# Optimization experiments

Hardware: AMD Instinct MI355X
Metric: run time of the kernel (lower is better)

The kernel has to match this reference:

```python
import jax, jax.numpy as jnp
import numpy as np

B, N, C, P, H = 4096, 14, 512, 1024, 8  # batch, seq(=seg_sz), in_ch, proj_ch, heads
D = P // H                               # dim_head = 128
SCALE = D ** -0.5
EPS = 1e-5


def setup_inputs() -> dict:
    key = jax.random.key(0)
    ks = jax.random.split(key, 12)
    inp = {
        "x1": jax.random.normal(ks[0], (B, N, C), jnp.float32),
        "x2": jax.random.normal(ks[1], (B, N, C), jnp.float32),
        # hr: external per-batch gate over attention scores, broadcast over heads
        "hr": jax.random.uniform(ks[2], (B, N, N), jnp.float32),
        # Embedding(in_ch*2 -> proj_ch-256), modeled as Linear
        "W_emb": jax.random.normal(ks[3], (2 * C, P - 256), jnp.float32) * (2 * C) ** -0.5,
        "b_emb": jnp.zeros((P - 256,), jnp.float32),
        # learned absolute positional embedding [N, 256]
        "pos": jax.random.normal(ks[4], (N, 256), jnp.float32) * 0.02,
        # qkv projection, no bias (bias=False in source)
        "W_qkv": jax.random.normal(ks[5], (P, 3 * P), jnp.float32) * P ** -0.5,
        # post-attention LayerNorm
        "ln_g": jnp.ones((P,), jnp.float32),
        "ln_b": jnp.zeros((P,), jnp.float32),
        # FeedForward(P -> 1.5P -> P)
        "W1": jax.random.normal(ks[6], (P, int(P * 1.5)), jnp.float32) * P ** -0.5,
        "b1": jnp.zeros((int(P * 1.5),), jnp.float32),
        "W2": jax.random.normal(ks[7], (int(P * 1.5), P), jnp.float32) * (int(P * 1.5)) ** -0.5,
        "b2": jnp.zeros((P,), jnp.float32),
    }
    return inp


def _layernorm(x, g, b):
    mu = jnp.mean(x, axis=-1, keepdims=True)
    var = jnp.mean(jnp.square(x - mu), axis=-1, keepdims=True)
    return (x - mu) * jax.lax.rsqrt(var + EPS) * g + b


def reference(x1, x2, hr, W_emb, b_emb, pos, W_qkv, ln_g, ln_b, W1, b1, W2, b2):
    x = jnp.concatenate([x1, x2], axis=-1)                    # [B,N,2C]
    e = x @ W_emb + b_emb                                     # [B,N,P-256]
    pe = jnp.broadcast_to(pos, (x.shape[0],) + pos.shape)     # [B,N,256]
    x = jnp.concatenate([e, pe], axis=-1)                     # [B,N,P]
    res = x
    qkv = x @ W_qkv                                           # [B,N,3P]
    q, k, v = jnp.split(qkv, 3, axis=-1)
    def split_heads(t):
        return t.reshape(t.shape[0], t.shape[1], H, D).transpose(0, 2, 1, 3)  # [B,H,N,D]
    q, k, v = split_heads(q), split_heads(k), split_heads(v)
    dots = jnp.einsum('bhid,bhjd->bhij', q, k) * SCALE        # [B,H,N,N]
    attn = jax.nn.softmax(dots, axis=-1) * hr[:, None]        # post-softmax multiplicative gate
    # dropout = identity (eval mode)
    o = jnp.einsum('bhij,bhjd->bhid', attn, v)                # [B,H,N,D]
    o = o.transpose(0, 2, 1, 3).reshape(o.shape[0], N, P)     # [B,N,P]
    x = _layernorm(o + res, ln_g, ln_b)
    x = jax.nn.gelu(x @ W1 + b1) @ W2 + b2                    # FeedForward (dropout=identity)
    return x
```

## Files before the change

### kernel.cpp

```cpp
#include <hip/hip_runtime.h>
#include <hip/hip_bf16.h>
#include <cstdint>
#include <cstddef>

using bf16 = __hip_bfloat16;

typedef __attribute__((ext_vector_type(8))) short short8;
typedef __attribute__((ext_vector_type(4))) float fx4;

#define MROWS 57344

__device__ __forceinline__ float b2f(bf16 v) { return __bfloat162float(v); }
__device__ __forceinline__ bf16  f2b(float v) { return __float2bfloat16(v); }

union U2B { uint2 u; bf16 h[4]; };
union U4B { uint4 u; bf16 h[8]; };

#define GL2LDS(g, l)                                                  \
  __builtin_amdgcn_global_load_lds(                                   \
      (__attribute__((address_space(1))) void*)(g),                   \
      (__attribute__((address_space(3))) void*)(l), 16, 0, 0)

__global__ void detect_k(const uint32_t* __restrict__ g, int* __restrict__ flag) {
  if (threadIdx.x == 0) *flag = ((g[0] & 0xFFFFu) == 0x3F80u) ? 1 : 0;
}

__device__ __forceinline__ float loadAs(const void* p, size_t i, bool isbf) {
  return isbf ? b2f(((const bf16*)p)[i]) : ((const float*)p)[i];
}

__global__ void cvt8_k(const void* __restrict__ src, bf16* __restrict__ dst,
                       int n8, const int* __restrict__ flag) {
  const int i = blockIdx.x * 256 + threadIdx.x;
  if (i >= n8) return;
  U4B o;
  if (*flag) {
    o.u = ((const uint4*)src)[i];
  } else {
    const float* f = (const float*)src + (size_t)i * 8;
#pragma unroll
    for (int j = 0; j < 8; ++j) o.h[j] = f2b(f[j]);
  }
  ((uint4*)dst)[i] = o.u;
}

__global__ void transpose_k(const void* __restrict__ W, bf16* __restrict__ Wt,
                            int K, int N, const int* __restrict__ flag) {
  __shared__ float s[32][33];
  const bool isbf = (*flag != 0);
  const int n0 = blockIdx.x * 32, k0 = blockIdx.y * 32;
  const int tx = threadIdx.x, ty = threadIdx.y;
  for (int i = ty; i < 32; i += 8)
    s[i][tx] = loadAs(W, (size_t)(k0 + i) * N + n0 + tx, isbf);
  __syncthreads();
  for (int i = ty; i < 32; i += 8)
    Wt[(size_t)(n0 + i) * K + k0 + tx] = f2b(s[tx][i]);
}

__global__ void concat_k(const void* __restrict__ x1, const void* __restrict__ x2,
                         bf16* __restrict__ xcat, const int* __restrict__ flag) {
  const int m = blockIdx.x, j = threadIdx.x;
  const bool isbf = (*flag != 0);
  const void* src = (j < 64) ? x1 : x2;
  const int jj = (j < 64) ? j : j - 64;
  U4B o;
  if (isbf) {
    o.u = *(const uint4*)((const bf16*)src + (size_t)m * 512 + jj * 8);
  } else {
    const float* f = (const float*)src + (size_t)m * 512 + jj * 8;
#pragma unroll
    for (int q = 0; q < 8; ++q) o.h[q] = f2b(f[q]);
  }
  *(uint4*)(xcat + (size_t)m * 1024 + j * 8) = o.u;
}

__global__ void posfill_k(const void* __restrict__ pos, bf16* __restrict__ xp,
                          const int* __restrict__ flag) {
  const int m = blockIdx.x, j = threadIdx.x;
  xp[(size_t)m * 1024 + 768 + j] = f2b(loadAs(pos, (m % 14) * 256 + j, *flag != 0));
}

template <int EPI, int OUTDT>
__global__ __launch_bounds__(256, 2)
void gemm_bt(const bf16* __restrict__ A, const bf16* __restrict__ Bt,
             void* __restrict__ C, const bf16* __restrict__ bias,
             const int* __restrict__ dtflag, int M, int N, int K, int ldc) {
  __shared__ bf16 smem[16384];
  bf16* a_s = smem;
  bf16* b_s = smem + 8192;

  const int t = threadIdx.x;
  const int w = t >> 6, L = t & 63, quad = L >> 4, l15 = L & 15;
  const int wr = w >> 1, wc = w & 1;
  const int m0 = blockIdx.y * 128, n0 = blockIdx.x * 128;
  const bool bfout = OUTDT ? (*dtflag != 0) : true;

  const int srow = L >> 2;
  const int scol = (L & 3) * 8;
  const bf16* gA = A + (size_t)(m0 + w * 32 + srow) * K + scol;
  const bf16* gB = Bt + (size_t)(n0 + w * 32 + srow) * K + scol;
  const size_t gstep = (size_t)16 * K;

  fx4 acc[4][4];
#pragma unroll
  for (int r = 0; r < 4; ++r)
#pragma unroll
    for (int c = 0; c < 4; ++c) acc[r][c] = fx4{0.f, 0.f, 0.f, 0.f};

  {
    bf16* lA = a_s + w * 1024;
    bf16* lB = b_s + w * 1024;
    GL2LDS(gA, lA);
    GL2LDS(gA + gstep, lA + 512);
    GL2LDS(gB, lB);
    GL2LDS(gB + gstep, lB + 512);
  }

  int cur = 0;
  for (int k0 = 0; k0 < K; k0 += 32) {
    const int nk = k0 + 32;
    if (nk < K) {
      bf16* lA = a_s + (cur ^ 1) * 4096 + w * 1024;
      bf16* lB = b_s + (cur ^ 1) * 4096 + w * 1024;
      GL2LDS(gA + nk, lA);
      GL2LDS(gA + gstep + nk, lA + 512);
      GL2LDS(gB + nk, lB);
      GL2LDS(gB + gstep + nk, lB + 512);
      asm volatile("s_waitcnt vmcnt(4)" ::: "memory");
    } else {
      asm volatile("s_waitcnt vmcnt(0)" ::: "memory");
    }
    __builtin_amdgcn_s_barrier();

    const bf16* as = a_s + cur * 4096;
    const bf16* bs = b_s + cur * 4096;
    short8 af[4], bfr[4];
#pragma unroll
    for (int r = 0; r < 4; ++r)
      af[r] = *(const short8*)(as + (wr * 64 + r * 16 + l15) * 32 + quad * 8);
#pragma unroll
    for (int c = 0; c < 4; ++c)
      bfr[c] = *(const short8*)(bs + (wc * 64 + c * 16 + l15) * 32 + quad * 8);
    asm volatile("s_waitcnt lgkmcnt(0)" ::: "memory");
    __builtin_amdgcn_sched_barrier(0);
#pragma unroll
    for (int r = 0; r < 4; ++r)
#pragma unroll
      for (int c = 0; c < 4; ++c)
        acc[r][c] = __builtin_amdgcn_mfma_f32_16x16x32_bf16(af[r], bfr[c],
                                                            acc[r][c], 0, 0, 0);
    asm volatile("" ::: "memory");
    __builtin_amdgcn_s_barrier();
    cur ^= 1;
  }

  float* eps = (float*)smem + (size_t)w * 1088;
  const int erow = L >> 2;
  const int ec0  = L & 3;

  float bv[4] = {0.f, 0.f, 0.f, 0.f};
  if (EPI >= 1) {
#pragma unroll
    for (int c = 0; c < 4; ++c) bv[c] = b2f(bias[n0 + wc * 64 + c * 16 + l15]);
  }

#pragma unroll
  for (int r = 0; r < 4; ++r) {
#pragma unroll
    for (int c = 0; c < 4; ++c) {
#pragma unroll
      for (int g = 0; g < 4; ++g) {
        float x = acc[r][c][g] + bv[c];
        if (EPI == 2)
          x = x / (1.f + __expf(-1.5957691216f * (x + 0.044715f * x * x * x)));
        eps[(quad * 4 + g) * 68 + c * 16 + l15] = x;
      }
    }
    asm volatile("s_waitcnt lgkmcnt(0)" ::: "memory");
    __builtin_amdgcn_sched_barrier(0);
    const int grow = m0 + wr * 64 + r * 16 + erow;
#pragma unroll
    for (int i = 0; i < 4; ++i) {
      const int cc = ec0 * 4 + i * 16;
      fx4 v = *(const fx4*)(eps + erow * 68 + cc);
      const size_t cbase = (size_t)grow * ldc + n0 + wc * 64 + cc;
      if (bfout) {
        U2B pk;
        pk.h[0] = f2b(v[0]); pk.h[1] = f2b(v[1]);
        pk.h[2] = f2b(v[2]); pk.h[3] = f2b(v[3]);
        *(uint2*)((bf16*)C + cbase) = pk.u;
      } else {
        *(fx4*)((float*)C + cbase) = v;
      }
    }
    __builtin_amdgcn_sched_barrier(0);
  }
}

__global__ __launch_bounds__(256)
void attn_ln_k(const bf16* __restrict__ qkv, const bf16* __restrict__ xp,
               const bf16* __restrict__ hr, const bf16* __restrict__ ln_g,
               const bf16* __restrict__ ln_b, bf16* __restrict__ y) {
  constexpr int LD = 2056;
  __shared__ bf16 s_qk[14 * LD];
  __shared__ bf16 s_P[8 * 16 * 16];
  __shared__ float s_red[4][14][2];
  __shared__ float s_stats[14][2];

  const int b = blockIdx.x;
  const int t = threadIdx.x;
  const int w = t >> 6, L = t & 63, quad = L >> 4, l15 = L & 15;
  const size_t qkv_base = (size_t)b * 14 * 3072;

  for (int c = t; c < 3584; c += 256) {
    const int i = c >> 8, off = (c & 255) * 8;
    *(uint4*)(s_qk + i * LD + off) =
        *(const uint4*)(qkv + qkv_base + (size_t)i * 3072 + off);
  }
  __syncthreads();

  const int iq = (l15 < 14) ? l15 : 13;
#pragma unroll
  for (int hh = 0; hh < 2; ++hh) {
    const int h = w * 2 + hh;
    fx4 acc = fx4{0.f, 0.f, 0.f, 0.f};
#pragma unroll
    for (int kk = 0; kk < 4; ++kk) {
      short8 aq = *(const short8*)(s_qk + iq * LD + h * 128 + kk * 32 + quad * 8);
      short8 bk = *(const short8*)(s_qk + iq * LD + 1024 + h * 128 + kk * 32 + quad * 8);
      acc = __builtin_amdgcn_mfma_f32_16x16x32_bf16(aq, bk, acc, 0, 0, 0);
    }
    const int j = l15;
#pragma unroll
    for (int r = 0; r < 4; ++r) {
      float s = acc[r] * 0.08838834764831845f;
      if (j >= 14) s = -1e9f;
      float m = s;
#pragma unroll
      for (int mask = 1; mask < 16; mask <<= 1)
        m = fmaxf(m, __shfl_xor(m, mask, 16));
      const float e = __expf(s - m);
      float ssum = e;
#pragma unroll
      for (int mask = 1; mask < 16; mask <<= 1) ssum += __shfl_xor(ssum, mask, 16);
      float pr = e / ssum;
      const int i = quad * 4 + r;
      float gv = 0.f;
      if (i < 14 && j < 14)
        gv = pr * b2f(hr[(size_t)b * 196 + i * 14 + j]);
      s_P[h * 256 + i * 16 + j] = f2b(gv);
    }
  }
  __syncthreads();

  const int h = t >> 5, sub = t & 31;
  const int col = h * 128 + sub * 4;
  fx4 o[14];
#pragma unroll
  for (int i = 0; i < 14; ++i) o[i] = fx4{0.f, 0.f, 0.f, 0.f};
  for (int j = 0; j < 14; ++j) {
    U2B vv;
    vv.u = *(const uint2*)(qkv + qkv_base + (size_t)j * 3072 + 2048 + col);
    const float v0 = b2f(vv.h[0]), v1 = b2f(vv.h[1]),
                v2 = b2f(vv.h[2]), v3 = b2f(vv.h[3]);
#pragma unroll
    for (int i = 0; i < 14; ++i) {
      const float pij = b2f(s_P[h * 256 + i * 16 + j]);
      o[i][0] += pij * v0;
      o[i][1] += pij * v1;
      o[i][2] += pij * v2;
      o[i][3] += pij * v3;
    }
  }

  float sm[14], sq[14];
#pragma unroll
  for (int i = 0; i < 14; ++i) {
    U2B rr;
    rr.u = *(const uint2*)(xp + ((size_t)b * 14 + i) * 1024 + col);
    o[i][0] += b2f(rr.h[0]);
    o[i][1] += b2f(rr.h[1]);
    o[i][2] += b2f(rr.h[2]);
    o[i][3] += b2f(rr.h[3]);
    sm[i] = o[i][0] + o[i][1] + o[i][2] + o[i][3];
    sq[i] = o[i][0] * o[i][0] + o[i][1] * o[i][1] + o[i][2] * o[i][2] +
            o[i][3] * o[i][3];
  }
#pragma unroll
  for (int i = 0; i < 14; ++i) {
#pragma unroll
    for (int mask = 1; mask < 64; mask <<= 1) {
      sm[i] += __shfl_xor(sm[i], mask, 64);
      sq[i] += __shfl_xor(sq[i], mask, 64);
    }
  }
  if (L == 0) {
#pragma unroll
    for (int i = 0; i < 14; ++i) {
      s_red[w][i][0] = sm[i];
      s_red[w][i][1] = sq[i];
    }
  }
  __syncthreads();
  if (t < 14) {
    float S = 0.f, Q = 0.f;
#pragma unroll
    for (int ww = 0; ww < 4; ++ww) {
      S += s_red[ww][t][0];
      Q += s_red[ww][t][1];
    }
    const float mu = S * (1.f / 1024.f);
    const float var = Q * (1.f / 1024.f) - mu * mu;
    s_stats[t][0] = mu;
    s_stats[t][1] = rsqrtf(fmaxf(var, 0.f) + 1e-5f);
  }
  __syncthreads();

  U2B gg, bb;
  gg.u = *(const uint2*)(ln_g + col);
  bb.u = *(const uint2*)(ln_b + col);
#pragma unroll
  for (int i = 0; i < 14; ++i) {
    const float mu = s_stats[i][0], rs = s_stats[i][1];
    U2B ov;
    ov.h[0] = f2b((o[i][0] - mu) * rs * b2f(gg.h[0]) + b2f(bb.h[0]));
    ov.h[1] = f2b((o[i][1] - mu) * rs * b2f(gg.h[1]) + b2f(bb.h[1]));
    ov.h[2] = f2b((o[i][2] - mu) * rs * b2f(gg.h[2]) + b2f(bb.h[2]));
    ov.h[3] = f2b((o[i][3] - mu) * rs * b2f(gg.h[3]) + b2f(bb.h[3]));
    *(uint2*)(y + ((size_t)b * 14 + i) * 1024 + col) = ov.u;
  }
}

extern "C" void kernel_launch(void* const* d_in, const int* in_sizes, int n_in,
                              void* d_out, int out_size, void* d_ws,
                              size_t ws_size, hipStream_t stream) {
  const void* x1    = d_in[0];
  const void* x2    = d_in[1];
  const void* hr    = d_in[2];
  const void* W_emb = d_in[3];
  const void* b_emb = d_in[4];
  const void* pos   = d_in[5];
  const void* W_qkv = d_in[6];
  const void* ln_g  = d_in[7];
  const void* ln_b  = d_in[8];
  const void* W1    = d_in[9];
  const void* b1    = d_in[10];
  const void* W2    = d_in[11];
  const void* b2    = d_in[12];

  bf16* ws = (bf16*)d_ws;
  int* flag = (int*)d_ws;
  size_t off = 8;
  auto alloc = [&](size_t n) { bf16* p = ws + off; off += n; return p; };
  bf16* WembT = alloc((size_t)768 * 1024);
  bf16* WqkvT = alloc((size_t)3072 * 1024);
  bf16* W1T   = alloc((size_t)1536 * 1024);
  bf16* W2T   = alloc((size_t)1024 * 1536);
  bf16* bembB = alloc(768);
  bf16* b1B   = alloc(1536);
  bf16* b2B   = alloc(1024);
  bf16* lngB  = alloc(1024);
  bf16* lnbB  = alloc(1024);
  bf16* hrB   = alloc((size_t)4096 * 196);
  bf16* xp    = alloc((size_t)MROWS * 1024);
  bf16* qkv   = alloc((size_t)MROWS * 3072);
  bf16* xcat  = qkv;
  bf16* mid   = qkv;
  bf16* yb    = (bf16*)d_out;

  detect_k<<<1, 64, 0, stream>>>((const uint32_t*)ln_g, flag);

  const dim3 tb(32, 8);
  transpose_k<<<dim3(768 / 32, 1024 / 32), tb, 0, stream>>>(W_emb, WembT, 1024, 768, flag);
  transpose_k<<<dim3(3072 / 32, 1024 / 32), tb, 0, stream>>>(W_qkv, WqkvT, 1024, 3072, flag);
  transpose_k<<<dim3(1536 / 32, 1024 / 32), tb, 0, stream>>>(W1, W1T, 1024, 1536, flag);
  transpose_k<<<dim3(1024 / 32, 1536 / 32), tb, 0, stream>>>(W2, W2T, 1536, 1024, flag);

  cvt8_k<<<1, 256, 0, stream>>>(b_emb, bembB, 96, flag);
  cvt8_k<<<1, 256, 0, stream>>>(b1, b1B, 192, flag);
  cvt8_k<<<1, 256, 0, stream>>>(b2, b2B, 128, flag);
  cvt8_k<<<1, 256, 0, stream>>>(ln_g, lngB, 128, flag);
  cvt8_k<<<1, 256, 0, stream>>>(ln_b, lnbB, 128, flag);
  cvt8_k<<<392, 256, 0, stream>>>(hr, hrB, 100352, flag);

  concat_k<<<MROWS, 128, 0, stream>>>(x1, x2, xcat, flag);
  posfill_k<<<MROWS, 256, 0, stream>>>(pos, xp, flag);

  gemm_bt<1, 0><<<dim3(6, MROWS / 128), 256, 0, stream>>>(
      xcat, WembT, xp, bembB, nullptr, MROWS, 768, 1024, 1024);
  gemm_bt<0, 0><<<dim3(24, MROWS / 128), 256, 0, stream>>>(
      xp, WqkvT, qkv, nullptr, nullptr, MROWS, 3072, 1024, 3072);
  attn_ln_k<<<4096, 256, 0, stream>>>(qkv, xp, hrB, lngB, lnbB, yb);
  gemm_bt<2, 0><<<dim3(12, MROWS / 128), 256, 0, stream>>>(
      yb, W1T, mid, b1B, nullptr, MROWS, 1536, 1024, 1536);
  gemm_bt<1, 1><<<dim3(8, MROWS / 128), 256, 0, stream>>>(
      mid, W2T, d_out, b2B, flag, MROWS, 1024, 1536, 1024);
}
```

Baseline: 2.067 ms.

## Replace GEMM with 256x256-tile 8-wave kernel using swizzled LDS and staged prefetch

```diff
diff --git a/kernel.cpp b/kernel.cpp
--- a/kernel.cpp
+++ b/kernel.cpp
@@ -81,109 +81,145 @@
 }
 
 template <int EPI, int OUTDT>
-__global__ __launch_bounds__(256, 2)
-void gemm_bt(const bf16* __restrict__ A, const bf16* __restrict__ Bt,
-             void* __restrict__ C, const bf16* __restrict__ bias,
-             const int* __restrict__ dtflag, int M, int N, int K, int ldc) {
-  __shared__ bf16 smem[16384];
-  bf16* a_s = smem;
-  bf16* b_s = smem + 8192;
+__global__ __launch_bounds__(512, 1)
+void gemm_bt8(const bf16* __restrict__ A, const bf16* __restrict__ Bt,
+              void* __restrict__ C, const bf16* __restrict__ bias,
+              const int* __restrict__ dtflag, int M, int N, int K, int ldc) {
+  __shared__ bf16 smem[65536];
+  char* sb = (char*)smem;
 
   const int t = threadIdx.x;
   const int w = t >> 6, L = t & 63, quad = L >> 4, l15 = L & 15;
-  const int wr = w >> 1, wc = w & 1;
-  const int m0 = blockIdx.y * 128, n0 = blockIdx.x * 128;
+  const int wr = w >> 2, wcn = w & 3;
+  const int m0 = blockIdx.y * 256, n0 = blockIdx.x * 256;
   const bool bfout = OUTDT ? (*dtflag != 0) : true;
 
-  const int srow = L >> 2;
-  const int scol = (L & 3) * 8;
-  const bf16* gA = A + (size_t)(m0 + w * 32 + srow) * K + scol;
-  const bf16* gB = Bt + (size_t)(n0 + w * 32 + srow) * K + scol;
-  const size_t gstep = (size_t)16 * K;
-
-  fx4 acc[4][4];
-#pragma unroll
-  for (int r = 0; r < 4; ++r)
+  int aoffk[2];
+#pragma unroll
+  for (int ks = 0; ks < 2; ++ks)
+    aoffk[ks] = (l15 * 128 + ks * 64 + quad * 16) ^ ((l15 & 7) << 4);
+
+  const int srow = w * 8 + (L >> 3);
+  const int scol = ((L & 7) ^ ((L >> 3) & 7)) * 8;
+  const bf16* gA = A + (size_t)(m0 + srow) * K + scol;
+  const bf16* gB = Bt + (size_t)(n0 + srow) * K + scol;
+  const int sdst = w * 1024;
+
+  auto stageA = [&](int buf, int h, int kt) {
+    const bf16* g = gA + (size_t)(h * 128) * K + (size_t)kt * 64;
+    char* d = sb + buf * 65536 + h * 16384 + sdst;
+    GL2LDS(g, d);
+    GL2LDS(g + (size_t)64 * K, d + 8192);
+  };
+  auto stageB = [&](int buf, int h, int kt) {
+    const bf16* g = gB + (size_t)(h * 128) * K + (size_t)kt * 64;
+    char* d = sb + buf * 65536 + 32768 + h * 16384 + sdst;
+    GL2LDS(g, d);
+    GL2LDS(g + (size_t)64 * K, d + 8192);
+  };
+
+  fx4 acc[8][4];
+#pragma unroll
+  for (int r = 0; r < 8; ++r)
 #pragma unroll
     for (int c = 0; c < 4; ++c) acc[r][c] = fx4{0.f, 0.f, 0.f, 0.f};
 
-  {
-    bf16* lA = a_s + w * 1024;
-    bf16* lB = b_s + w * 1024;
-    GL2LDS(gA, lA);
-    GL2LDS(gA + gstep, lA + 512);
-    GL2LDS(gB, lB);
-    GL2LDS(gB + gstep, lB + 512);
-  }
-
-  int cur = 0;
-  for (int k0 = 0; k0 < K; k0 += 32) {
-    const int nk = k0 + 32;
-    if (nk < K) {
-      bf16* lA = a_s + (cur ^ 1) * 4096 + w * 1024;
-      bf16* lB = b_s + (cur ^ 1) * 4096 + w * 1024;
-      GL2LDS(gA + nk, lA);
-      GL2LDS(gA + gstep + nk, lA + 512);
-      GL2LDS(gB + nk, lB);
-      GL2LDS(gB + gstep + nk, lB + 512);
-      asm volatile("s_waitcnt vmcnt(4)" ::: "memory");
-    } else {
-      asm volatile("s_waitcnt vmcnt(0)" ::: "memory");
-    }
-    __builtin_amdgcn_s_barrier();
-
-    const bf16* as = a_s + cur * 4096;
-    const bf16* bs = b_s + cur * 4096;
-    short8 af[4], bfr[4];
-#pragma unroll
-    for (int r = 0; r < 4; ++r)
-      af[r] = *(const short8*)(as + (wr * 64 + r * 16 + l15) * 32 + quad * 8);
-#pragma unroll
-    for (int c = 0; c < 4; ++c)
-      bfr[c] = *(const short8*)(bs + (wc * 64 + c * 16 + l15) * 32 + quad * 8);
+  stageA(0, 0, 0); stageA(0, 1, 0);
+  stageB(0, 0, 0); stageB(0, 1, 0);
+  stageB(1, 0, 1); stageB(1, 1, 1);
+  asm volatile("s_waitcnt vmcnt(4)" ::: "memory");
+  __builtin_amdgcn_s_barrier();
+
+  const int NI = K >> 7;
+  for (int i = 0; i < NI; ++i) {
+    const bool more = (i < NI - 1);
+    const int kt1 = 2 * i + 1, ktn = 2 * i + 2;
+
+#pragma unroll
+    for (int half = 0; half < 2; ++half) {
+      const int ab = half * 65536 + wr * 16384;
+      const int bb = half * 65536 + 32768 + (wcn >> 1) * 16384 + (wcn & 1) * 8192;
+      short8 bfr[4][2];
+#pragma unroll
+      for (int q = 0; q < 4; ++q) {
+        const int p = half * 4 + q;
+        if (q == 0) {
+#pragma unroll
+          for (int fc = 0; fc < 4; ++fc)
+#pragma unroll
+            for (int ks = 0; ks < 2; ++ks)
+              bfr[fc][ks] = *(const short8*)(sb + bb + fc * 2048 + aoffk[ks]);
+        }
+        short8 af[2][2];
+#pragma unroll
+        for (int rr = 0; rr < 2; ++rr)
+#pragma unroll
+          for (int ks = 0; ks < 2; ++ks)
+            af[rr][ks] =
+                *(const short8*)(sb + ab + (2 * q + rr) * 2048 + aoffk[ks]);
+        if (p == 0)      stageA(1, 0, kt1);
+        else if (p == 1) stageA(1, 1, kt1);
+        else if (more) {
+          if (p == 2)      stageB(0, 0, ktn);
+          else if (p == 3) stageB(0, 1, ktn);
+          else if (p == 4) stageA(0, 0, ktn);
+          else if (p == 5) stageA(0, 1, ktn);
+          else if (p == 6) stageB(1, 0, ktn + 1);
+          else             stageB(1, 1, ktn + 1);
+        }
+        if (p == 3) {
+          if (more) asm volatile("s_waitcnt vmcnt(4)" ::: "memory");
+          else      asm volatile("s_waitcnt vmcnt(0)" ::: "memory");
+        } else if (p == 7) {
+          if (more) asm volatile("s_waitcnt vmcnt(4)" ::: "memory");
+        }
+        __builtin_amdgcn_s_barrier();
+        asm volatile("s_waitcnt lgkmcnt(0)" ::: "memory");
+        __builtin_amdgcn_sched_barrier(0);
+        __builtin_amdgcn_s_setprio(1);
+#pragma unroll
+        for (int fc = 0; fc < 4; ++fc)
+#pragma unroll
+          for (int rr = 0; rr < 2; ++rr)
+#pragma unroll
+            for (int ks = 0; ks < 2; ++ks)
+              acc[2 * q + rr][fc] = __builtin_amdgcn_mfma_f32_16x16x32_bf16(
+                  af[rr][ks], bfr[fc][ks], acc[2 * q + rr][fc], 0, 0, 0);
+        __builtin_amdgcn_s_setprio(0);
+        __builtin_amdgcn_sched_barrier(0);
+        __builtin_amdgcn_s_barrier();
+      }
+    }
+  }
+
+  float* eps = (float*)sb + (size_t)w * 1088;
+  const int erow = L >> 2, ec0 = L & 3;
+  float bv[4] = {0.f, 0.f, 0.f, 0.f};
+  if (EPI >= 1) {
+#pragma unroll
+    for (int fc = 0; fc < 4; ++fc)
+      bv[fc] = b2f(bias[n0 + wcn * 64 + fc * 16 + l15]);
+  }
+
+#pragma unroll
+  for (int fr = 0; fr < 8; ++fr) {
+#pragma unroll
+    for (int fc = 0; fc < 4; ++fc)
+#pragma unroll
+      for (int g = 0; g < 4; ++g) {
+        float x = acc[fr][fc][g] + bv[fc];
+        if (EPI == 2)
+          x = x / (1.f + __expf(-1.5957691216f * (x + 0.044715f * x * x * x)));
+        eps[(quad * 4 + g) * 68 + fc * 16 + l15] = x;
+      }
     asm volatile("s_waitcnt lgkmcnt(0)" ::: "memory");
     __builtin_amdgcn_sched_barrier(0);
-#pragma unroll
-    for (int r = 0; r < 4; ++r)
-#pragma unroll
-      for (int c = 0; c < 4; ++c)
-        acc[r][c] = __builtin_amdgcn_mfma_f32_16x16x32_bf16(af[r], bfr[c],
-                                                            acc[r][c], 0, 0, 0);
-    asm volatile("" ::: "memory");
-    __builtin_amdgcn_s_barrier();
-    cur ^= 1;
-  }
-
-  float* eps = (float*)smem + (size_t)w * 1088;
-  const int erow = L >> 2;
-  const int ec0  = L & 3;
-
-  float bv[4] = {0.f, 0.f, 0.f, 0.f};
-  if (EPI >= 1) {
-#pragma unroll
-    for (int c = 0; c < 4; ++c) bv[c] = b2f(bias[n0 + wc * 64 + c * 16 + l15]);
-  }
-
-#pragma unroll
-  for (int r = 0; r < 4; ++r) {
-#pragma unroll
-    for (int c = 0; c < 4; ++c) {
-#pragma unroll
-      for (int g = 0; g < 4; ++g) {
-        float x = acc[r][c][g] + bv[c];
-        if (EPI == 2)
-          x = x / (1.f + __expf(-1.5957691216f * (x + 0.044715f * x * x * x)));
-        eps[(quad * 4 + g) * 68 + c * 16 + l15] = x;
-      }
-    }
-    asm volatile("s_waitcnt lgkmcnt(0)" ::: "memory");
-    __builtin_amdgcn_sched_barrier(0);
-    const int grow = m0 + wr * 64 + r * 16 + erow;
-#pragma unroll
-    for (int i = 0; i < 4; ++i) {
-      const int cc = ec0 * 4 + i * 16;
+    const int grow = m0 + wr * 128 + fr * 16 + erow;
+#pragma unroll
+    for (int i2 = 0; i2 < 4; ++i2) {
+      const int cc = ec0 * 4 + i2 * 16;
       fx4 v = *(const fx4*)(eps + erow * 68 + cc);
-      const size_t cbase = (size_t)grow * ldc + n0 + wc * 64 + cc;
+      const size_t cbase = (size_t)grow * ldc + n0 + wcn * 64 + cc;
       if (bfout) {
         U2B pk;
         pk.h[0] = f2b(v[0]); pk.h[1] = f2b(v[1]);
@@ -386,13 +422,13 @@
   concat_k<<<MROWS, 128, 0, stream>>>(x1, x2, xcat, flag);
   posfill_k<<<MROWS, 256, 0, stream>>>(pos, xp, flag);
 
-  gemm_bt<1, 0><<<dim3(6, MROWS / 128), 256, 0, stream>>>(
+  gemm_bt8<1, 0><<<dim3(3, 224), 512, 0, stream>>>(
       xcat, WembT, xp, bembB, nullptr, MROWS, 768, 1024, 1024);
-  gemm_bt<0, 0><<<dim3(24, MROWS / 128), 256, 0, stream>>>(
+  gemm_bt8<0, 0><<<dim3(12, 224), 512, 0, stream>>>(
       xp, WqkvT, qkv, nullptr, nullptr, MROWS, 3072, 1024, 3072);
   attn_ln_k<<<4096, 256, 0, stream>>>(qkv, xp, hrB, lngB, lnbB, yb);
-  gemm_bt<2, 0><<<dim3(12, MROWS / 128), 256, 0, stream>>>(
+  gemm_bt8<2, 0><<<dim3(6, 224), 512, 0, stream>>>(
       yb, W1T, mid, b1B, nullptr, MROWS, 1536, 1024, 1536);
-  gemm_bt<1, 1><<<dim3(8, MROWS / 128), 256, 0, stream>>>(
+  gemm_bt8<1, 1><<<dim3(4, 224), 512, 0, stream>>>(
       mid, W2T, d_out, b2B, flag, MROWS, 1024, 1536, 1024);
 }
```

Result: faster. 1.698 ms (-17.8%).
